# Performance work log

Hardware: AMD Instinct MI355X
Metric: run time of the kernel (lower is better)

Reference implementation:

```python
import jax, jax.numpy as jnp
import numpy as np

D = 1024
H = 16
HD = D // H


def setup_inputs() -> dict:
    key = jax.random.key(0)
    ks = jax.random.split(key, 9)
    s = 1.0 / np.sqrt(D)
    inp = {
        "x": jax.random.normal(ks[0], (2, 2048, D), dtype=jnp.float32),
        "Wq": jax.random.uniform(ks[1], (D, D), jnp.float32, -s, s),
        "bq": jax.random.uniform(ks[2], (D,), jnp.float32, -s, s),
        "Wk": jax.random.uniform(ks[3], (D, D), jnp.float32, -s, s),
        "bk": jax.random.uniform(ks[4], (D,), jnp.float32, -s, s),
        "Wv": jax.random.uniform(ks[5], (D, D), jnp.float32, -s, s),
        "bv": jax.random.uniform(ks[6], (D,), jnp.float32, -s, s),
        "Wo": jax.random.uniform(ks[7], (D, D), jnp.float32, -s, s),
        "bo": jax.random.uniform(ks[8], (D,), jnp.float32, -s, s),
    }
    return inp


def reference(x, Wq, bq, Wk, bk, Wv, bv, Wo, bo):
    B, S, _ = x.shape
    scale = jnp.sqrt(jnp.asarray(HD, dtype=jnp.float32))
    # QKV projections, split into heads: [B, H, S, HD]
    def proj(W, b):
        y = jnp.einsum('bsd,de->bse', x, W) + b
        return y.reshape(B, S, H, HD).transpose(0, 2, 1, 3)
    Q, K, V = proj(Wq, bq), proj(Wk, bk), proj(Wv, bv)
    scores = jnp.einsum('bhqd,bhkd->bhqk', Q, K) / scale  # [B,H,S,S]
    attn = jax.nn.softmax(scores, axis=-1)
    ctx = jnp.einsum('bhqk,bhkd->bhqd', attn, V)
    ctx = ctx.transpose(0, 2, 1, 3).reshape(B, S, D)
    return jnp.einsum('bsd,de->bse', ctx, Wo) + bo
```

## Files before the change

kernel.cpp:

```cpp
#include <hip/hip_runtime.h>
#include <hip/hip_bf16.h>

typedef __attribute__((ext_vector_type(8))) _Float16 f16x8;
typedef __attribute__((ext_vector_type(4))) float f32x4;

constexpr int Sc  = 2048;
constexpr int Dc  = 1024;
constexpr int Hc  = 16;
constexpr int HDc = 64;
constexpr int Mc  = 4096;

constexpr float ECs = 0.18033688011112042f;

__device__ __forceinline__ ushort f2h(float f) {
  return __builtin_bit_cast(ushort, (_Float16)f);
}

__device__ __forceinline__ void glds16(const ushort* g, ushort* l) {
  __builtin_amdgcn_global_load_lds(
      (const __attribute__((address_space(1))) unsigned int*)(g),
      (__attribute__((address_space(3))) unsigned int*)(l), 16, 0, 0);
}

union US8 {
  ushort u[8];
  uint   w[4];
  f16x8  v;
};

struct SplitP {
  const float* W[4];
  ushort*      Th[4];
};

__global__ __launch_bounds__(256) void prep_kernel(
    const float* __restrict__ X, ushort* __restrict__ Xh, SplitP p) {
  __shared__ float T[64][69];
  const int wid = blockIdx.x;
  const int t   = threadIdx.x;
  if (wid < 4096) {
    const int i    = wid * 256 + t;
    const float4 v = ((const float4*)X)[i];
    ushort4 h;
    h.x = f2h(v.x);
    h.y = f2h(v.y);
    h.z = f2h(v.z);
    h.w = f2h(v.w);
    ((ushort4*)Xh)[i] = h;
    return;
  }
  const int w2 = wid - 4096;
  const int z  = w2 >> 8;
  const int by = (w2 >> 4) & 15;
  const int bx = w2 & 15;
  const float* W = p.W[z];
  const int c  = (t & 15) * 4;
  const int r  = t >> 4;
  const int n0 = bx * 64, k0 = by * 64;
#pragma unroll
  for (int pp = 0; pp < 4; ++pp) {
    const int k    = r + pp * 16;
    const float4 v = *(const float4*)(W + (size_t)(k0 + k) * 1024 + n0 + c);
    T[k][c + 0] = v.x;
    T[k][c + 1] = v.y;
    T[k][c + 2] = v.z;
    T[k][c + 3] = v.w;
  }
  __syncthreads();
#pragma unroll
  for (int pp = 0; pp < 4; ++pp) {
    const int n = r + pp * 16;
    ushort4 h;
    h.x = f2h(T[c + 0][n]);
    h.y = f2h(T[c + 1][n]);
    h.z = f2h(T[c + 2][n]);
    h.w = f2h(T[c + 3][n]);
    *(ushort4*)(p.Th[z] + (size_t)(n0 + n) * 1024 + k0 + c) = h;
  }
}

struct GemmP {
  const ushort* Bh[3];
  const float*  bias[3];
  void*         Out[3];
};

template <bool QKV>
__global__ __launch_bounds__(256) void gemm_f16(
    const ushort* __restrict__ A, GemmP p) {
  __shared__ __align__(16) ushort As[2][128 * 32];
  __shared__ __align__(16) ushort Bs[2][128 * 32];

  const int t  = threadIdx.x;
  const int z  = blockIdx.z;
  const int m0 = blockIdx.x * 128, n0 = blockIdx.y * 128;
  const ushort* Bh  = p.Bh[z];
  const float* bias = p.bias[z];

  const int lane = t & 63, wave = t >> 6;
  const int wm = (wave & 1) * 64, wn = (wave >> 1) * 64;

  f32x4 acc[4][4];
#pragma unroll
  for (int i = 0; i < 4; ++i)
#pragma unroll
    for (int j = 0; j < 4; ++j) acc[i][j] = (f32x4){0.f, 0.f, 0.f, 0.f};

  const int am = wave * 16 + (lane >> 2);
  const int q  = ((lane & 3) - (am >> 1)) & 3;
  const ushort* gA = A  + (size_t)(m0 + am) * 1024 + q * 8;
  const ushort* gB = Bh + (size_t)(n0 + am) * 1024 + q * 8;
  const int ls0 = wave * 512;
  const int ls1 = 2048 + wave * 512;

  const int fr  = lane & 15;
  const int fkb = (((lane >> 4) + (fr >> 1)) & 3) * 16;

  glds16(gA,             &As[0][ls0]);
  glds16(gA + 64 * 1024, &As[0][ls1]);
  glds16(gB,             &Bs[0][ls0]);
  glds16(gB + 64 * 1024, &Bs[0][ls1]);

  int bp = 0;
  for (int k0 = 0; k0 < 1024; k0 += 32) {
    __syncthreads();
    if (k0 + 32 < 1024) {
      glds16(gA + k0 + 32,             &As[bp ^ 1][ls0]);
      glds16(gA + k0 + 32 + 64 * 1024, &As[bp ^ 1][ls1]);
      glds16(gB + k0 + 32,             &Bs[bp ^ 1][ls0]);
      glds16(gB + k0 + 32 + 64 * 1024, &Bs[bp ^ 1][ls1]);
    }

    f16x8 a[4], b_h[4];
#pragma unroll
    for (int i = 0; i < 4; ++i) {
      const int ra = (wm + i * 16 + fr) * 64 + fkb;
      const int rb = (wn + i * 16 + fr) * 64 + fkb;
      a[i]   = *(const f16x8*)((const char*)As[bp] + ra);
      b_h[i] = *(const f16x8*)((const char*)Bs[bp] + rb);
    }
#pragma unroll
    for (int i = 0; i < 4; ++i)
#pragma unroll
      for (int j = 0; j < 4; ++j)
        acc[i][j] = __builtin_amdgcn_mfma_f32_16x16x32_f16(a[i], b_h[j], acc[i][j], 0, 0, 0);
    bp ^= 1;
  }

  const float osc = (QKV && z == 0) ? ECs : 1.0f;
  const int cr = (lane >> 4) * 4;
  const int cc = lane & 15;
#pragma unroll
  for (int j = 0; j < 4; ++j) {
    const int n    = n0 + wn + j * 16 + cc;
    const float bv = bias[n];
#pragma unroll
    for (int i = 0; i < 4; ++i) {
      const int mb = m0 + wm + i * 16 + cr;
#pragma unroll
      for (int r = 0; r < 4; ++r) {
        const int m   = mb + r;
        const float v = (acc[i][j][r] + bv) * osc;
        if (QKV) {
          const int b = m >> 11, s = m & 2047, h = n >> 6, hd = n & 63;
          ((ushort*)p.Out[z])[(((size_t)(b * Hc + h) * Sc + s) << 6) + hd] = f2h(v);
        } else {
          ((float*)p.Out[z])[(size_t)m * 1024 + n] = v;
        }
      }
    }
  }
}

__global__ __launch_bounds__(256, 2) void attn_mfma3(
    const ushort* __restrict__ Q, const ushort* __restrict__ K,
    const ushort* __restrict__ V, ushort* __restrict__ CTX) {
  __shared__ __align__(16) ushort Ks[64 * 64];
  __shared__ __align__(16) ushort Vt[64 * 64];

  const int t    = threadIdx.x;
  const int lane = t & 63, wave = t >> 6;
  const int c16 = lane & 15, quad = lane >> 4;
  const int wg = blockIdx.x;
  const int bh = wg & 31, qt = wg >> 5;
  const int bb = bh >> 4, hh = bh & 15;

  const ushort* Qb = Q + (size_t)bh * Sc * HDc + (size_t)qt * 256 * HDc;
  const ushort* Kb = K + (size_t)bh * Sc * HDc;
  const ushort* Vb = V + (size_t)bh * Sc * HDc;

  f16x8 aq[2][2][2];
#pragma unroll
  for (int qh = 0; qh < 2; ++qh)
#pragma unroll
    for (int mt = 0; mt < 2; ++mt)
#pragma unroll
      for (int c = 0; c < 2; ++c)
        aq[qh][mt][c] = *(const f16x8*)(Qb +
            (size_t)(wave * 64 + qh * 32 + mt * 16 + c16) * 64 + c * 32 + quad * 8);

  US8 ones_u;
#pragma unroll
  for (int e = 0; e < 8; ++e) ones_u.u[e] = 0x3C00;
  const f16x8 ones = ones_u.v;
  const f32x4 kZ = (f32x4){0.f, 0.f, 0.f, 0.f};

  f32x4 ctx[2][2][4], lacc[2][2];
#pragma unroll
  for (int qh = 0; qh < 2; ++qh)
#pragma unroll
    for (int mt = 0; mt < 2; ++mt) {
      lacc[qh][mt] = (f32x4){0.f, 0.f, 0.f, 0.f};
#pragma unroll
      for (int j = 0; j < 4; ++j) ctx[qh][mt][j] = (f32x4){0.f, 0.f, 0.f, 0.f};
    }

  const int fslot = ((quad + (c16 >> 1)) & 3) * 8;

  const int krow = t >> 2, kac = t & 3;
  const int kl = krow * 64 + ((kac + (krow >> 1)) & 3) * 8;

  const int kg = t & 15, dg = t >> 4;
  const int vc   = (kg >> 3) * 32;
  const int vq   = kg & 3;
  const int vsub = ((kg >> 2) & 1) * 4;

  const ushort* gK = Kb + (size_t)krow * 64 + kac * 8;
  const ushort* gV = Vb + (size_t)(kg * 4) * 64 + dg * 4;

  f16x8 kr0, kr1;
  ushort4 vr[4];
  kr0 = *(const f16x8*)(gK);
  kr1 = *(const f16x8*)(gK + 32);
#pragma unroll
  for (int i = 0; i < 4; ++i) vr[i] = *(const ushort4*)(gV + (size_t)i * 64);

  for (int kt = 0; kt < 32; ++kt) {
    __syncthreads();
    *(f16x8*)&Ks[kl]      = kr0;
    *(f16x8*)&Ks[kl + 32] = kr1;
    {
      const uint* w0 = (const uint*)&vr[0];
      const uint* w1 = (const uint*)&vr[1];
      const uint* w2 = (const uint*)&vr[2];
      const uint* w3 = (const uint*)&vr[3];
#pragma unroll
      for (int j = 0; j < 4; ++j) {
        const int  wd  = j >> 1;
        const uint sel = (j & 1) ? 0x07060302u : 0x05040100u;
        const uint lo  = __builtin_amdgcn_perm(w1[wd], w0[wd], sel);
        const uint hi  = __builtin_amdgcn_perm(w3[wd], w2[wd], sel);
        const int row  = dg * 4 + j;
        const int slot = (vq + (row >> 1)) & 3;
        *(uint2*)&Vt[row * 64 + vc + slot * 8 + vsub] = make_uint2(lo, hi);
      }
    }
    __syncthreads();

    if (kt < 31) {
      const size_t adv = (size_t)(kt + 1) * 64 * 64;
      kr0 = *(const f16x8*)(gK + adv);
      kr1 = *(const f16x8*)(gK + adv + 32);
#pragma unroll
      for (int i = 0; i < 4; ++i) vr[i] = *(const ushort4*)(gV + adv + (size_t)i * 64);
    }

#pragma unroll
    for (int qh = 0; qh < 2; ++qh) {
      f32x4 st[2][4];
      __builtin_amdgcn_s_setprio(1);
#pragma unroll
      for (int j = 0; j < 4; ++j) {
        const f16x8 ak0 = *(const f16x8*)&Ks[(j * 16 + c16) * 64 + fslot];
        st[0][j] = __builtin_amdgcn_mfma_f32_16x16x32_f16(ak0, aq[qh][0][0], kZ, 0, 0, 0);
        st[1][j] = __builtin_amdgcn_mfma_f32_16x16x32_f16(ak0, aq[qh][1][0], kZ, 0, 0, 0);
      }
#pragma unroll
      for (int j = 0; j < 4; ++j) {
        const f16x8 ak1 = *(const f16x8*)&Ks[(j * 16 + c16) * 64 + 32 + fslot];
        st[0][j] = __builtin_amdgcn_mfma_f32_16x16x32_f16(ak1, aq[qh][0][1], st[0][j], 0, 0, 0);
        st[1][j] = __builtin_amdgcn_mfma_f32_16x16x32_f16(ak1, aq[qh][1][1], st[1][j], 0, 0, 0);
      }
      __builtin_amdgcn_s_setprio(0);

      US8 pf[2][2];
#pragma unroll
      for (int mt = 0; mt < 2; ++mt)
#pragma unroll
        for (int c2 = 0; c2 < 2; ++c2)
#pragma unroll
          for (int w = 0; w < 4; ++w) {
            const int jj = c2 * 2 + (w >> 1);
            const int r0 = (w & 1) * 2;
            const float pe = __builtin_amdgcn_exp2f(st[mt][jj][r0]);
            const float po = __builtin_amdgcn_exp2f(st[mt][jj][r0 + 1]);
            const auto pk = __builtin_amdgcn_cvt_pkrtz(pe, po);
            pf[mt][c2].w[w] = __builtin_bit_cast(uint, pk);
          }

      __builtin_amdgcn_s_setprio(1);
#pragma unroll
      for (int c2 = 0; c2 < 2; ++c2) {
        lacc[qh][0] = __builtin_amdgcn_mfma_f32_16x16x32_f16(pf[0][c2].v, ones, lacc[qh][0], 0, 0, 0);
        lacc[qh][1] = __builtin_amdgcn_mfma_f32_16x16x32_f16(pf[1][c2].v, ones, lacc[qh][1], 0, 0, 0);
#pragma unroll
        for (int j = 0; j < 4; ++j) {
          const f16x8 bv = *(const f16x8*)&Vt[(j * 16 + c16) * 64 + c2 * 32 + fslot];
          ctx[qh][0][j] = __builtin_amdgcn_mfma_f32_16x16x32_f16(pf[0][c2].v, bv, ctx[qh][0][j], 0, 0, 0);
          ctx[qh][1][j] = __builtin_amdgcn_mfma_f32_16x16x32_f16(pf[1][c2].v, bv, ctx[qh][1][j], 0, 0, 0);
        }
      }
      __builtin_amdgcn_s_setprio(0);
    }
  }

#pragma unroll
  for (int qh = 0; qh < 2; ++qh)
#pragma unroll
    for (int mt = 0; mt < 2; ++mt) {
#pragma unroll
      for (int r = 0; r < 4; ++r) {
        const float inv = 1.f / lacc[qh][mt][r];
        const int srow  = qt * 256 + wave * 64 + qh * 32 + mt * 16 + quad * 4 + r;
        const size_t rb = ((size_t)(bb * Sc + srow)) * 1024 + hh * 64;
#pragma unroll
        for (int j = 0; j < 4; ++j)
          CTX[rb + j * 16 + c16] = f2h(ctx[qh][mt][j][r] * inv);
      }
    }
}

extern "C" void kernel_launch(void* const* d_in, const int* in_sizes, int n_in,
                              void* d_out, int out_size, void* d_ws, size_t ws_size,
                              hipStream_t stream) {
  (void)in_sizes; (void)n_in; (void)out_size; (void)ws_size;
  const float* x  = (const float*)d_in[0];
  const float* Wq = (const float*)d_in[1];
  const float* bq = (const float*)d_in[2];
  const float* Wk = (const float*)d_in[3];
  const float* bk = (const float*)d_in[4];
  const float* Wv = (const float*)d_in[5];
  const float* bv = (const float*)d_in[6];
  const float* Wo = (const float*)d_in[7];
  const float* bo = (const float*)d_in[8];

  const size_t MB = 1024 * 1024;
  char* w    = (char*)d_ws;
  ushort* Qw  = (ushort*)(w + 0 * MB);
  ushort* Kw  = (ushort*)(w + 8 * MB);
  ushort* Vw  = (ushort*)(w + 16 * MB);
  ushort* Cw  = (ushort*)(w + 24 * MB);
  ushort* Xh  = (ushort*)(w + 32 * MB);
  ushort* WT  = (ushort*)(w + 40 * MB);
  ushort* Whq = WT + 0 * 1048576;
  ushort* Whk = WT + 1 * 1048576;
  ushort* Whv = WT + 2 * 1048576;
  ushort* Who = WT + 3 * 1048576;

  const dim3 blk(256);

  SplitP sp;
  sp.W[0] = Wq; sp.W[1] = Wk; sp.W[2] = Wv; sp.W[3] = Wo;
  sp.Th[0] = Whq; sp.Th[1] = Whk; sp.Th[2] = Whv; sp.Th[3] = Who;
  prep_kernel<<<dim3(5120), blk, 0, stream>>>(x, Xh, sp);

  GemmP pq;
  pq.Bh[0] = Whq; pq.Bh[1] = Whk; pq.Bh[2] = Whv;
  pq.bias[0] = bq; pq.bias[1] = bk; pq.bias[2] = bv;
  pq.Out[0] = Qw; pq.Out[1] = Kw; pq.Out[2] = Vw;
  gemm_f16<true><<<dim3(Mc / 128, Dc / 128, 3), blk, 0, stream>>>(Xh, pq);

  attn_mfma3<<<dim3(256), blk, 0, stream>>>(Qw, Kw, Vw, Cw);

  GemmP po;
  po.Bh[0] = po.Bh[1] = po.Bh[2] = Who;
  po.bias[0] = po.bias[1] = po.bias[2] = bo;
  po.Out[0] = po.Out[1] = po.Out[2] = d_out;
  gemm_f16<false><<<dim3(Mc / 128, Dc / 128, 1), blk, 0, stream>>>(Cw, po);
}
```

Measured before the change: 185.5 us.

## Load K fragments directly into registers and overlap V transpose with QK^T

```diff
diff --git a/kernel.cpp b/kernel.cpp
--- a/kernel.cpp
+++ b/kernel.cpp
@@ -175,7 +175,6 @@
 __global__ __launch_bounds__(256, 2) void attn_mfma3(
     const ushort* __restrict__ Q, const ushort* __restrict__ K,
     const ushort* __restrict__ V, ushort* __restrict__ CTX) {
-  __shared__ __align__(16) ushort Ks[64 * 64];
   __shared__ __align__(16) ushort Vt[64 * 64];
 
   const int t    = threadIdx.x;
@@ -217,28 +216,26 @@
 
   const int fslot = ((quad + (c16 >> 1)) & 3) * 8;
 
-  const int krow = t >> 2, kac = t & 3;
-  const int kl = krow * 64 + ((kac + (krow >> 1)) & 3) * 8;
-
   const int kg = t & 15, dg = t >> 4;
   const int vc   = (kg >> 3) * 32;
   const int vq   = kg & 3;
   const int vsub = ((kg >> 2) & 1) * 4;
-
-  const ushort* gK = Kb + (size_t)krow * 64 + kac * 8;
   const ushort* gV = Vb + (size_t)(kg * 4) * 64 + dg * 4;
 
-  f16x8 kr0, kr1;
+  const ushort* gKf = Kb + (size_t)c16 * 64 + quad * 8;
+
+  f16x8 kf[4][2];
+#pragma unroll
+  for (int j = 0; j < 4; ++j) {
+    kf[j][0] = *(const f16x8*)(gKf + (size_t)(j * 16) * 64);
+    kf[j][1] = *(const f16x8*)(gKf + (size_t)(j * 16) * 64 + 32);
+  }
   ushort4 vr[4];
-  kr0 = *(const f16x8*)(gK);
-  kr1 = *(const f16x8*)(gK + 32);
 #pragma unroll
   for (int i = 0; i < 4; ++i) vr[i] = *(const ushort4*)(gV + (size_t)i * 64);
 
   for (int kt = 0; kt < 32; ++kt) {
     __syncthreads();
-    *(f16x8*)&Ks[kl]      = kr0;
-    *(f16x8*)&Ks[kl + 32] = kr1;
     {
       const uint* w0 = (const uint*)&vr[0];
       const uint* w1 = (const uint*)&vr[1];
@@ -255,35 +252,24 @@
         *(uint2*)&Vt[row * 64 + vc + slot * 8 + vsub] = make_uint2(lo, hi);
       }
     }
-    __syncthreads();
-
-    if (kt < 31) {
-      const size_t adv = (size_t)(kt + 1) * 64 * 64;
-      kr0 = *(const f16x8*)(gK + adv);
-      kr1 = *(const f16x8*)(gK + adv + 32);
-#pragma unroll
-      for (int i = 0; i < 4; ++i) vr[i] = *(const ushort4*)(gV + adv + (size_t)i * 64);
-    }
-
+
+    US8 pf[2][2][2];
 #pragma unroll
     for (int qh = 0; qh < 2; ++qh) {
       f32x4 st[2][4];
       __builtin_amdgcn_s_setprio(1);
 #pragma unroll
       for (int j = 0; j < 4; ++j) {
-        const f16x8 ak0 = *(const f16x8*)&Ks[(j * 16 + c16) * 64 + fslot];
-        st[0][j] = __builtin_amdgcn_mfma_f32_16x16x32_f16(ak0, aq[qh][0][0], kZ, 0, 0, 0);
-        st[1][j] = __builtin_amdgcn_mfma_f32_16x16x32_f16(ak0, aq[qh][1][0], kZ, 0, 0, 0);
+        st[0][j] = __builtin_amdgcn_mfma_f32_16x16x32_f16(kf[j][0], aq[qh][0][0], kZ, 0, 0, 0);
+        st[1][j] = __builtin_amdgcn_mfma_f32_16x16x32_f16(kf[j][0], aq[qh][1][0], kZ, 0, 0, 0);
       }
 #pragma unroll
       for (int j = 0; j < 4; ++j) {
-        const f16x8 ak1 = *(const f16x8*)&Ks[(j * 16 + c16) * 64 + 32 + fslot];
-        st[0][j] = __builtin_amdgcn_mfma_f32_16x16x32_f16(ak1, aq[qh][0][1], st[0][j], 0, 0, 0);
-        st[1][j] = __builtin_amdgcn_mfma_f32_16x16x32_f16(ak1, aq[qh][1][1], st[1][j], 0, 0, 0);
+        st[0][j] = __builtin_amdgcn_mfma_f32_16x16x32_f16(kf[j][1], aq[qh][0][1], st[0][j], 0, 0, 0);
+        st[1][j] = __builtin_amdgcn_mfma_f32_16x16x32_f16(kf[j][1], aq[qh][1][1], st[1][j], 0, 0, 0);
       }
       __builtin_amdgcn_s_setprio(0);
 
-      US8 pf[2][2];
 #pragma unroll
       for (int mt = 0; mt < 2; ++mt)
 #pragma unroll
@@ -295,23 +281,39 @@
             const float pe = __builtin_amdgcn_exp2f(st[mt][jj][r0]);
             const float po = __builtin_amdgcn_exp2f(st[mt][jj][r0 + 1]);
             const auto pk = __builtin_amdgcn_cvt_pkrtz(pe, po);
-            pf[mt][c2].w[w] = __builtin_bit_cast(uint, pk);
+            pf[qh][mt][c2].w[w] = __builtin_bit_cast(uint, pk);
           }
-
-      __builtin_amdgcn_s_setprio(1);
+    }
+
+    __syncthreads();
+
+    if (kt < 31) {
+      const size_t adv = (size_t)(kt + 1) * 64 * 64;
+#pragma unroll
+      for (int j = 0; j < 4; ++j) {
+        kf[j][0] = *(const f16x8*)(gKf + adv + (size_t)(j * 16) * 64);
+        kf[j][1] = *(const f16x8*)(gKf + adv + (size_t)(j * 16) * 64 + 32);
+      }
+#pragma unroll
+      for (int i = 0; i < 4; ++i) vr[i] = *(const ushort4*)(gV + adv + (size_t)i * 64);
+    }
+
+    __builtin_amdgcn_s_setprio(1);
+#pragma unroll
+    for (int qh = 0; qh < 2; ++qh) {
 #pragma unroll
       for (int c2 = 0; c2 < 2; ++c2) {
-        lacc[qh][0] = __builtin_amdgcn_mfma_f32_16x16x32_f16(pf[0][c2].v, ones, lacc[qh][0], 0, 0, 0);
-        lacc[qh][1] = __builtin_amdgcn_mfma_f32_16x16x32_f16(pf[1][c2].v, ones, lacc[qh][1], 0, 0, 0);
+        lacc[qh][0] = __builtin_amdgcn_mfma_f32_16x16x32_f16(pf[qh][0][c2].v, ones, lacc[qh][0], 0, 0, 0);
+        lacc[qh][1] = __builtin_amdgcn_mfma_f32_16x16x32_f16(pf[qh][1][c2].v, ones, lacc[qh][1], 0, 0, 0);
 #pragma unroll
         for (int j = 0; j < 4; ++j) {
           const f16x8 bv = *(const f16x8*)&Vt[(j * 16 + c16) * 64 + c2 * 32 + fslot];
-          ctx[qh][0][j] = __builtin_amdgcn_mfma_f32_16x16x32_f16(pf[0][c2].v, bv, ctx[qh][0][j], 0, 0, 0);
-          ctx[qh][1][j] = __builtin_amdgcn_mfma_f32_16x16x32_f16(pf[1][c2].v, bv, ctx[qh][1][j], 0, 0, 0);
+          ctx[qh][0][j] = __builtin_amdgcn_mfma_f32_16x16x32_f16(pf[qh][0][c2].v, bv, ctx[qh][0][j], 0, 0, 0);
+          ctx[qh][1][j] = __builtin_amdgcn_mfma_f32_16x16x32_f16(pf[qh][1][c2].v, bv, ctx[qh][1][j], 0, 0, 0);
         }
       }
-      __builtin_amdgcn_s_setprio(0);
-    }
+    }
+    __builtin_amdgcn_s_setprio(0);
   }
 
 #pragma unroll
```

After: 209.2 us. +12.8%, slower.
